# Performance work log

Hardware: AMD Instinct MI355X
Metric: run time of the kernel (lower is better)

## Reference

```python
import jax, jax.numpy as jnp
import numpy as np
import math

H = 768          # bert hidden size
N_HYPO = 384     # number of hyponym instance embeddings
N_HYPER = 384    # number of hypernym instance embeddings
NUM_LABELS = 3


def setup_inputs() -> dict:
    key = jax.random.key(0)
    k1, k2, k3 = jax.random.split(key, 3)
    return {
        "hypo_embeddings": jax.random.normal(k1, (N_HYPO, H), dtype=jnp.float32),
        "hyper_embeddings": jax.random.normal(k2, (N_HYPER, H), dtype=jnp.float32),
        "W_cls": jax.random.normal(k3, (NUM_LABELS, 4 * H), dtype=jnp.float32) * 0.02,
        "b_cls": jnp.zeros((NUM_LABELS,), dtype=jnp.float32),
    }


def reference(hypo_embeddings, hyper_embeddings, W_cls, b_cls):
    h = hypo_embeddings.shape[-1]
    inv_sqrt_h = 1.0 / math.sqrt(h)
    # elementwise outer-product attention score: tanh(x_i * y_j) summed over hidden
    # [n_hypo, n_hyper, h] intermediate -> [n_hypo, n_hyper]
    att = jnp.tanh(hypo_embeddings[:, None, :] * hyper_embeddings[None, :, :]).sum(-1) * inv_sqrt_h

    hypo_side_att = jax.nn.softmax(att, axis=-1)   # rows attend over hypers
    hyper_side_att = jax.nn.softmax(att, axis=0)   # cols attend over hypos

    hyper_typ = hypo_side_att.sum(axis=0)
    hyper_typ = hyper_typ / hyper_typ.sum()
    hypo_typ = hyper_side_att.sum(axis=-1)
    hypo_typ = hypo_typ / hypo_typ.sum()

    # typicalness-weighted prototype pooling
    hyper_prototype = jnp.einsum('nm,md,n->d', hypo_side_att, hyper_embeddings, hypo_typ)
    hypo_prototype = jnp.einsum('nm,nd,m->d', hyper_side_att, hypo_embeddings, hyper_typ)

    feats = jnp.concatenate([
        hyper_prototype,
        hypo_prototype,
        hyper_prototype - hypo_prototype,
        hyper_prototype * hypo_prototype,
    ])  # [4h]
    sub_pred = W_cls @ feats + b_cls  # [num_labels]
    return sub_pred
```

## Files before the change

### kernel.cpp

```cpp
#include <hip/hip_runtime.h>
#include <hip/hip_bf16.h>

#define NN 384
#define HH 768
#define L2E 1.4426950408889634f
#define TWO_L2E 2.8853900817779268f
#define INV_SQRT_H 0.03608439182435161f

__device__ __forceinline__ float exp2_hw(float x) { return __builtin_amdgcn_exp2f(x); }
__device__ __forceinline__ float rcp_hw(float x) { return __builtin_amdgcn_rcpf(x); }

__global__ __launch_bounds__(256) void k_att(const float* __restrict__ X,
                                             const float* __restrict__ Y,
                                             float* __restrict__ att) {
    __shared__ float xs[8 * HH];
    __shared__ float ys[8 * HH];
    const int tid = threadIdx.x;
    const int i0 = blockIdx.y * 8, j0 = blockIdx.x * 8;

    const float4* gx = (const float4*)(X + i0 * HH);
    const float4* gy = (const float4*)(Y + j0 * HH);
    float4* xs4 = (float4*)xs;
    float4* ys4 = (float4*)ys;
#pragma unroll
    for (int p = 0; p < 6; p++) {
        int e = tid + p * 256;
        float4 vx = gx[e];
        float4 vy = gy[e];
        xs4[e] = vx;
        vy.x *= TWO_L2E; vy.y *= TWO_L2E; vy.z *= TWO_L2E; vy.w *= TWO_L2E;
        ys4[e] = vy;
    }
    __syncthreads();

    const int wv = tid >> 6, ln = tid & 63;
    for (int q = 0; q < 16; q++) {
        int p = wv * 16 + q;
        const float4* xr = (const float4*)(xs + (p >> 3) * HH);
        const float4* yr = (const float4*)(ys + (p & 7) * HH);
        float acc = 0.f;
#pragma unroll
        for (int m = 0; m < 3; m++) {
            float4 a = xr[m * 64 + ln];
            float4 b = yr[m * 64 + ln];
            acc += rcp_hw(exp2_hw(a.x * b.x) + 1.f);
            acc += rcp_hw(exp2_hw(a.y * b.y) + 1.f);
            acc += rcp_hw(exp2_hw(a.z * b.z) + 1.f);
            acc += rcp_hw(exp2_hw(a.w * b.w) + 1.f);
        }
#pragma unroll
        for (int o = 32; o; o >>= 1) acc += __shfl_xor(acc, o, 64);
        if (ln == 0) {
            att[(i0 + (p >> 3)) * NN + (j0 + (p & 7))] = (768.f - 2.f * acc) * INV_SQRT_H;
        }
    }
}

__global__ __launch_bounds__(256) void k_stats(const float* __restrict__ att, float* rowM,
                                               float* rowRS, float* colM, float* colRS) {
    __shared__ float red[4];
    int b = blockIdx.x, t = threadIdx.x;
    bool isRow = b < NN;
    int x = isRow ? b : b - NN;
    float a0 = isRow ? att[x * NN + t] : att[t * NN + x];
    float a1 = (t < 128) ? (isRow ? att[x * NN + t + 256] : att[(t + 256) * NN + x]) : -1e30f;
    float m = fmaxf(a0, a1);
#pragma unroll
    for (int o = 32; o; o >>= 1) m = fmaxf(m, __shfl_xor(m, o, 64));
    if ((t & 63) == 0) red[t >> 6] = m;
    __syncthreads();
    float M = fmaxf(fmaxf(red[0], red[1]), fmaxf(red[2], red[3]));
    __syncthreads();
    float s = exp2_hw((a0 - M) * L2E);
    if (t < 128) s += exp2_hw((a1 - M) * L2E);
#pragma unroll
    for (int o = 32; o; o >>= 1) s += __shfl_xor(s, o, 64);
    if ((t & 63) == 0) red[t >> 6] = s;
    __syncthreads();
    if (t == 0) {
        float S = (red[0] + red[1]) + (red[2] + red[3]);
        if (isRow) { rowM[x] = M; rowRS[x] = 1.f / S; }
        else       { colM[x] = M; colRS[x] = 1.f / S; }
    }
}

__global__ __launch_bounds__(256) void k_typ(const float* __restrict__ att,
                                             const float* __restrict__ rowM,
                                             const float* __restrict__ rowRS,
                                             const float* __restrict__ colM,
                                             const float* __restrict__ colRS,
                                             float* hyper_typ, float* hypo_typ) {
    __shared__ float red[4];
    int b = blockIdx.x, t = threadIdx.x;
    bool isCol = b < NN;
    int x = isCol ? b : b - NN;
    float s = 0.f;
    if (isCol) {
        int j = x;
        for (int i = t; i < NN; i += 256)
            s += exp2_hw((att[i * NN + j] - rowM[i]) * L2E) * rowRS[i];
    } else {
        int i = x;
        for (int j = t; j < NN; j += 256)
            s += exp2_hw((att[i * NN + j] - colM[j]) * L2E) * colRS[j];
    }
#pragma unroll
    for (int o = 32; o; o >>= 1) s += __shfl_xor(s, o, 64);
    if ((t & 63) == 0) red[t >> 6] = s;
    __syncthreads();
    if (t == 0) {
        float S = (red[0] + red[1]) + (red[2] + red[3]);
        if (isCol) hyper_typ[x] = S * (1.f / NN);
        else       hypo_typ[x]  = S * (1.f / NN);
    }
}

__global__ __launch_bounds__(256) void k_w(const float* __restrict__ att,
                                           const float* __restrict__ rowM,
                                           const float* __restrict__ rowRS,
                                           const float* __restrict__ colM,
                                           const float* __restrict__ colRS,
                                           const float* __restrict__ hypo_typ,
                                           const float* __restrict__ hyper_typ,
                                           float* w_hyper, float* w_hypo) {
    __shared__ float red[4];
    int b = blockIdx.x, t = threadIdx.x;
    bool isCol = b < NN;
    int x = isCol ? b : b - NN;
    float s = 0.f;
    if (isCol) {
        int j = x;
        for (int i = t; i < NN; i += 256)
            s += exp2_hw((att[i * NN + j] - rowM[i]) * L2E) * rowRS[i] * hypo_typ[i];
    } else {
        int i = x;
        for (int j = t; j < NN; j += 256)
            s += exp2_hw((att[i * NN + j] - colM[j]) * L2E) * colRS[j] * hyper_typ[j];
    }
#pragma unroll
    for (int o = 32; o; o >>= 1) s += __shfl_xor(s, o, 64);
    if ((t & 63) == 0) red[t >> 6] = s;
    __syncthreads();
    if (t == 0) {
        float S = (red[0] + red[1]) + (red[2] + red[3]);
        if (isCol) w_hyper[x] = S;
        else       w_hypo[x]  = S;
    }
}

__global__ __launch_bounds__(256) void k_proto(const float* __restrict__ X,
                                               const float* __restrict__ Y,
                                               const float* __restrict__ w_hyper,
                                               const float* __restrict__ w_hypo,
                                               float* hp, float* hq) {
    __shared__ float red[4][64];
    int b = blockIdx.x, t = threadIdx.x;
    bool hyper = b < 12;
    int bb = hyper ? b : b - 12;
    int dl = t & 63, w = t >> 6;
    int d = bb * 64 + dl;
    float s = 0.f;
    if (hyper) {
        for (int j = w * 96; j < w * 96 + 96; j++) s += w_hyper[j] * Y[j * HH + d];
    } else {
        for (int i = w * 96; i < w * 96 + 96; i++) s += w_hypo[i] * X[i * HH + d];
    }
    red[w][dl] = s;
    __syncthreads();
    if (t < 64) {
        float S = red[0][t] + red[1][t] + red[2][t] + red[3][t];
        if (hyper) hp[bb * 64 + t] = S;
        else       hq[bb * 64 + t] = S;
    }
}

__global__ __launch_bounds__(256) void k_cls(const float* __restrict__ W,
                                             const float* __restrict__ bias,
                                             const float* __restrict__ hp,
                                             const float* __restrict__ hq,
                                             float* __restrict__ out) {
    __shared__ float red[3][4];
    int t = threadIdx.x;
    float acc0 = 0.f, acc1 = 0.f, acc2 = 0.f;
    for (int d = t; d < 4 * HH; d += 256) {
        int seg = d / HH, r = d - seg * HH;
        float f = (seg == 0) ? hp[r] : (seg == 1) ? hq[r] : (seg == 2) ? (hp[r] - hq[r]) : (hp[r] * hq[r]);
        acc0 += W[d] * f;
        acc1 += W[3072 + d] * f;
        acc2 += W[6144 + d] * f;
    }
#pragma unroll
    for (int o = 32; o; o >>= 1) {
        acc0 += __shfl_xor(acc0, o, 64);
        acc1 += __shfl_xor(acc1, o, 64);
        acc2 += __shfl_xor(acc2, o, 64);
    }
    if ((t & 63) == 0) {
        red[0][t >> 6] = acc0;
        red[1][t >> 6] = acc1;
        red[2][t >> 6] = acc2;
    }
    __syncthreads();
    if (t < 3) {
        float S = red[t][0] + red[t][1] + red[t][2] + red[t][3] + bias[t];
        out[t] = S;
    }
}

extern "C" void kernel_launch(void* const* d_in, const int* in_sizes, int n_in,
                              void* d_out, int out_size, void* d_ws, size_t ws_size,
                              hipStream_t stream) {
    const float* X = (const float*)d_in[0];
    const float* Y = (const float*)d_in[1];
    const float* W = (const float*)d_in[2];
    const float* B = (const float*)d_in[3];
    float* out = (float*)d_out;

    float* ws = (float*)d_ws;
    float* att       = ws;
    float* rowM      = att + NN * NN;
    float* rowRS     = rowM + NN;
    float* colM      = rowRS + NN;
    float* colRS     = colM + NN;
    float* hyper_typ = colRS + NN;
    float* hypo_typ  = hyper_typ + NN;
    float* w_hyper   = hypo_typ + NN;
    float* w_hypo    = w_hyper + NN;
    float* hp        = w_hypo + NN;
    float* hq        = hp + HH;

    k_att<<<dim3(48, 48), 256, 0, stream>>>(X, Y, att);
    k_stats<<<768, 256, 0, stream>>>(att, rowM, rowRS, colM, colRS);
    k_typ<<<768, 256, 0, stream>>>(att, rowM, rowRS, colM, colRS, hyper_typ, hypo_typ);
    k_w<<<768, 256, 0, stream>>>(att, rowM, rowRS, colM, colRS, hypo_typ, hyper_typ, w_hyper, w_hypo);
    k_proto<<<24, 256, 0, stream>>>(X, Y, w_hyper, w_hypo, hp, hq);
    k_cls<<<1, 256, 0, stream>>>(W, B, hp, hq, out);
}
```

Baseline: 113.3 us.

## Remap att kernel so each lane owns an output pair, padding shared rows

Restructures the attention-score kernel so each of 64 lanes computes one (i,j) pair over a quarter of the hidden dimension. The four wave partials are then combined through shared memory. This replaces 16 sequential 64-lane shuffle reductions per wave with a single shared-memory reduction, and adds four independent accumulators for ILP. Shared rows are padded to 772 floats to avoid the bank conflicts the new strided per-lane access pattern would otherwise cause.

```diff
diff --git a/kernel.cpp b/kernel.cpp
--- a/kernel.cpp
+++ b/kernel.cpp
@@ -3,6 +3,7 @@
 
 #define NN 384
 #define HH 768
+#define HP 772
 #define L2E 1.4426950408889634f
 #define TWO_L2E 2.8853900817779268f
 #define INV_SQRT_H 0.03608439182435161f
@@ -13,46 +14,46 @@
 __global__ __launch_bounds__(256) void k_att(const float* __restrict__ X,
                                              const float* __restrict__ Y,
                                              float* __restrict__ att) {
-    __shared__ float xs[8 * HH];
-    __shared__ float ys[8 * HH];
+    __shared__ float xs[8 * HP];
+    __shared__ float ys[8 * HP];
+    __shared__ float part[4][64];
     const int tid = threadIdx.x;
     const int i0 = blockIdx.y * 8, j0 = blockIdx.x * 8;
 
     const float4* gx = (const float4*)(X + i0 * HH);
     const float4* gy = (const float4*)(Y + j0 * HH);
-    float4* xs4 = (float4*)xs;
-    float4* ys4 = (float4*)ys;
 #pragma unroll
     for (int p = 0; p < 6; p++) {
         int e = tid + p * 256;
+        int r = e / 192, c = e - r * 192;
         float4 vx = gx[e];
         float4 vy = gy[e];
-        xs4[e] = vx;
+        ((float4*)(xs + r * HP))[c] = vx;
         vy.x *= TWO_L2E; vy.y *= TWO_L2E; vy.z *= TWO_L2E; vy.w *= TWO_L2E;
-        ys4[e] = vy;
+        ((float4*)(ys + r * HP))[c] = vy;
     }
     __syncthreads();
 
     const int wv = tid >> 6, ln = tid & 63;
-    for (int q = 0; q < 16; q++) {
-        int p = wv * 16 + q;
-        const float4* xr = (const float4*)(xs + (p >> 3) * HH);
-        const float4* yr = (const float4*)(ys + (p & 7) * HH);
-        float acc = 0.f;
-#pragma unroll
-        for (int m = 0; m < 3; m++) {
-            float4 a = xr[m * 64 + ln];
-            float4 b = yr[m * 64 + ln];
-            acc += rcp_hw(exp2_hw(a.x * b.x) + 1.f);
-            acc += rcp_hw(exp2_hw(a.y * b.y) + 1.f);
-            acc += rcp_hw(exp2_hw(a.z * b.z) + 1.f);
-            acc += rcp_hw(exp2_hw(a.w * b.w) + 1.f);
-        }
-#pragma unroll
-        for (int o = 32; o; o >>= 1) acc += __shfl_xor(acc, o, 64);
-        if (ln == 0) {
-            att[(i0 + (p >> 3)) * NN + (j0 + (p & 7))] = (768.f - 2.f * acc) * INV_SQRT_H;
-        }
+    const int i = ln >> 3, j = ln & 7;
+    const float4* xr = (const float4*)(xs + i * HP) + wv * 48;
+    const float4* yr = (const float4*)(ys + j * HP) + wv * 48;
+    float a0 = 0.f, a1 = 0.f, a2 = 0.f, a3 = 0.f;
+#pragma unroll 8
+    for (int m = 0; m < 48; m++) {
+        float4 a = xr[m];
+        float4 b = yr[m];
+        a0 += rcp_hw(exp2_hw(a.x * b.x) + 1.f);
+        a1 += rcp_hw(exp2_hw(a.y * b.y) + 1.f);
+        a2 += rcp_hw(exp2_hw(a.z * b.z) + 1.f);
+        a3 += rcp_hw(exp2_hw(a.w * b.w) + 1.f);
+    }
+    part[wv][ln] = (a0 + a1) + (a2 + a3);
+    __syncthreads();
+    if (tid < 64) {
+        float s = part[0][tid] + part[1][tid] + part[2][tid] + part[3][tid];
+        int ii = tid >> 3, jj = tid & 7;
+        att[(i0 + ii) * NN + (j0 + jj)] = (768.f - 2.f * s) * INV_SQRT_H;
     }
 }
 
```

New measurement: 103.2 us. -8.9%, faster.
